# Kernel tuning notes

Measured on AMD Instinct MI355X. Metric: run time of the kernel, lower is better.

Reference implementation:

```python
import jax, jax.numpy as jnp
import numpy as np

EPS = 1e-7            # keras.backend.epsilon()
NEG = -1e30           # log-space 'zero' (avoid -inf for NaN-free grads)
SUB_SAMPLE = (2, 2)   # encoder conv subsampling factors (non-tensor forward arg)


def setup_inputs() -> dict:
    key = jax.random.key(0)
    k1, k2, k3, k4 = jax.random.split(key, 4)
    B, T, C, L = 128, 2000, 128, 200
    logits = jax.random.normal(k1, (B, T, C), jnp.float32)
    y_pred = jax.nn.softmax(logits, axis=-1)  # ctc_batch_cost expects probabilities
    labels = jax.random.randint(k2, (B, L), 0, C - 1, jnp.int32)  # never the blank (C-1)
    # raw frame counts; after two /2 subsamplings -> in [1000, 2000] <= T
    feat_lens = jax.random.randint(k3, (B,), 4000, 8000, jnp.int32)
    label_lens = jax.random.randint(k4, (B,), 50, L + 1, jnp.int32)
    return {"y_pred": y_pred, "labels": labels, "feat_lens": feat_lens, "label_lens": label_lens}


def _ctc_batch_cost(y_pred, labels, feat_lens, label_lens):
    """Faithful reimplementation of keras.backend.ctc_batch_cost (blank = C-1),
    with the CTCLayer's subsampling of feat_lens applied first."""
    for sub in SUB_SAMPLE:
        if sub > 1:
            feat_lens = (feat_lens + 1) // sub
    log_probs = jnp.log(y_pred + EPS)                 # [B,T,C]
    B, T, C = y_pred.shape
    L = labels.shape[1]
    S = 2 * L + 1
    blank = C - 1

    # extended label sequence: blank, l1, blank, l2, ..., blank  -> [B,S]
    ext = jnp.full((B, S), blank, jnp.int32).at[:, 1::2].set(labels)
    # skip transition s-2 -> s allowed iff ext[s] != blank and ext[s] != ext[s-2]
    skip_ok = jnp.concatenate(
        [jnp.zeros((B, 2), bool), (ext[:, 2:] != blank) & (ext[:, 2:] != ext[:, :-2])],
        axis=1,
    )
    bidx = jnp.arange(B)
    i1 = 2 * label_lens - 1   # last non-blank state
    i2 = 2 * label_lens       # trailing blank state

    lp = jnp.swapaxes(log_probs, 0, 1)                # [T,B,C], scan over time

    emit0 = jnp.take_along_axis(lp[0], ext, axis=1)   # [B,S]
    alpha0 = (jnp.full((B, S), NEG, jnp.float32)
              .at[:, 0].set(emit0[:, 0])
              .at[:, 1].set(emit0[:, 1]))
    ll0 = jnp.logaddexp(alpha0[bidx, i1], alpha0[bidx, i2])
    final0 = jnp.where(feat_lens == 1, ll0, NEG)

    def step(carry, inp):
        alpha, final = carry
        t, lp_t = inp
        emit = jnp.take_along_axis(lp_t, ext, axis=1)              # [B,S]
        a1 = jnp.pad(alpha, ((0, 0), (1, 0)), constant_values=NEG)[:, :-1]
        a2 = jnp.pad(alpha, ((0, 0), (2, 0)), constant_values=NEG)[:, :-2]
        m = jnp.logaddexp(alpha, a1)
        m = jnp.where(skip_ok, jnp.logaddexp(m, a2), m)
        alpha = m + emit
        ll = jnp.logaddexp(alpha[bidx, i1], alpha[bidx, i2])
        final = jnp.where(t == feat_lens - 1, ll, final)           # capture at last valid frame
        return (alpha, final), None

    (_, final), _ = jax.lax.scan(step, (alpha0, final0), (jnp.arange(1, T), lp[1:]))
    return -final[:, None]                                          # [B,1] like ctc_batch_cost


def reference(y_pred, labels, feat_lens, label_lens):
    return _ctc_batch_cost(y_pred, labels, feat_lens, label_lens)
```

## Files before the change

kernel.cpp:

```cpp
#include <hip/hip_runtime.h>
#include <math.h>

#define EPSQ 1e-7f
#define TDIM 2000
#define CDIM 128
#define LDIM 200
#define SDIM 401
#define SPL  7
#define SENTE (-(1 << 30))

#define RINGA 0
#define RINGB 8192
#define LABSI 16384
#define PRODA 16592
#define CONSA 16593
#define PRODB 16594
#define CONSB 16595
#define BDONE 16596
#define BVALS 16608
#define BEXPI 17056
#define SMEMN 17120

__device__ __forceinline__ float dpp_shr_f(float x) {
    return __int_as_float(__builtin_amdgcn_update_dpp(0, __float_as_int(x), 0x138, 0xf, 0xf, true));
}
__device__ __forceinline__ int dpp_shr_i(int x) {
    return __builtin_amdgcn_update_dpp(0, x, 0x138, 0xf, 0xf, true);
}
__device__ __forceinline__ float dpp_shl_f(float x) {
    return __int_as_float(__builtin_amdgcn_update_dpp(0, __float_as_int(x), 0x130, 0xf, 0xf, true));
}
__device__ __forceinline__ int dpp_shl_i(int x) {
    return __builtin_amdgcn_update_dpp(0, x, 0x130, 0xf, 0xf, true);
}

__device__ __forceinline__ void renorm_alpha(float a[SPL], int& E, float& fprev, int lane) {
    float mx = fmaxf(fmaxf(fmaxf(a[0], a[1]), fmaxf(a[2], a[3])),
                     fmaxf(fmaxf(a[4], a[5]), a[6]));
    bool zero = (mx == 0.f);
    int e = ((__float_as_int(mx) >> 23) & 0xff) - 127;
    int S_self = zero ? SENTE : (E + e);
    int S1 = dpp_shr_i(S_self);
    if (lane == 0) S1 = SENTE;
    int S2 = dpp_shr_i(S1);
    if (lane == 0) S2 = SENTE;
    int E_new = max(S_self, S1);
    int E_prevnew = max(S1, S2);
    int dg = E - E_new;
    float g = (zero || dg < -126) ? 0.f : __int_as_float((dg + 127) << 23);
#pragma unroll
    for (int j = 0; j < SPL; ++j) a[j] *= g;
    E = E_new;
    int df = E_prevnew - E_new;
    bool fz = (E_prevnew <= SENTE / 2) || (df < -126);
    if (df > 126) df = 126;
    fprev = fz ? 0.f : __int_as_float((df + 127) << 23);
}

__device__ __forceinline__ void renorm_beta(float b[SPL], int& E, float& fnext, int lane) {
    float mx = fmaxf(fmaxf(fmaxf(b[0], b[1]), fmaxf(b[2], b[3])),
                     fmaxf(fmaxf(b[4], b[5]), b[6]));
    bool zero = (mx == 0.f);
    int e = ((__float_as_int(mx) >> 23) & 0xff) - 127;
    int S_self = zero ? SENTE : (E + e);
    int S1 = dpp_shl_i(S_self);
    if (lane == 63) S1 = SENTE;
    int S2 = dpp_shl_i(S1);
    if (lane == 63) S2 = SENTE;
    int E_new = max(S_self, S1);
    int E_nextnew = max(S1, S2);
    int dg = E - E_new;
    float g = (zero || dg < -126) ? 0.f : __int_as_float((dg + 127) << 23);
#pragma unroll
    for (int j = 0; j < SPL; ++j) b[j] *= g;
    E = E_new;
    int df = E_nextnew - E_new;
    bool fz = (E_nextnew <= SENTE / 2) || (df < -126);
    if (df > 126) df = 126;
    fnext = fz ? 0.f : __int_as_float((df + 127) << 23);
}

#define A_STEP(TOFF) do {                                                     \
    float p6 = dpp_shr_f(a[6]) * fprev;                                       \
    float p5 = dpp_shr_f(a[5]) * fprev;                                       \
    float n0 = fmaf(skipf[0], p5,   a[0] + p6)   * q[(1+(TOFF))&3][0];        \
    float n1 = fmaf(skipf[1], p6,   a[1] + a[0]) * q[(1+(TOFF))&3][1];        \
    float n2 = fmaf(skipf[2], a[0], a[2] + a[1]) * q[(1+(TOFF))&3][2];        \
    float n3 = fmaf(skipf[3], a[1], a[3] + a[2]) * q[(1+(TOFF))&3][3];        \
    float n4 = fmaf(skipf[4], a[2], a[4] + a[3]) * q[(1+(TOFF))&3][4];        \
    float n5 = fmaf(skipf[5], a[3], a[5] + a[4]) * q[(1+(TOFF))&3][5];        \
    float n6 = fmaf(skipf[6], a[4], a[6] + a[5]) * q[(1+(TOFF))&3][6];        \
    a[0]=n0; a[1]=n1; a[2]=n2; a[3]=n3; a[4]=n4; a[5]=n5; a[6]=n6;            \
    if (t + (TOFF) == m) {                                                    \
        _Pragma("unroll")                                                     \
        for (int j = 0; j < SPL; ++j) ac[j] = a[j];                           \
        Eac = E;                                                              \
    }                                                                         \
    {   const int rr = ((t + (TOFF) + 2) & 63) << 7;                          \
        _Pragma("unroll")                                                     \
        for (int j = 0; j < SPL; ++j)                                         \
            q[(3+(TOFF))&3][j] = ringA[rr + cls[j]];                          \
    }                                                                         \
} while (0);

#define B_STEP(SOFF) do {                                                     \
    float c0 = bb[0]*q[(SOFF)&3][0], c1 = bb[1]*q[(SOFF)&3][1];               \
    float c2 = bb[2]*q[(SOFF)&3][2], c3 = bb[3]*q[(SOFF)&3][3];               \
    float c4 = bb[4]*q[(SOFF)&3][4], c5 = bb[5]*q[(SOFF)&3][5];               \
    float c6 = bb[6]*q[(SOFF)&3][6];                                          \
    float cn0 = dpp_shl_f(c0) * fnext;                                        \
    float cn1 = dpp_shl_f(c1) * fnext;                                        \
    bb[0] = fmaf(skb[0], c2, c0 + c1);                                        \
    bb[1] = fmaf(skb[1], c3, c1 + c2);                                        \
    bb[2] = fmaf(skb[2], c4, c2 + c3);                                        \
    bb[3] = fmaf(skb[3], c5, c3 + c4);                                        \
    bb[4] = fmaf(skb[4], c6, c4 + c5);                                        \
    bb[5] = fmaf(skb[5], cn0, c5 + c6);                                       \
    bb[6] = fmaf(skb[6], cn1, c6 + cn0);                                      \
    if (s + (SOFF) == scap) {                                                 \
        _Pragma("unroll")                                                     \
        for (int j = 0; j < SPL; ++j) bc[j] = bb[j];                          \
        Ebc = E;                                                              \
    }                                                                         \
    {   const int rr = ((t0 - s - (SOFF) - 2) & 63) << 7;                     \
        _Pragma("unroll")                                                     \
        for (int j = 0; j < SPL; ++j)                                         \
            q[(2+(SOFF))&3][j] = ringB[rr + cls[j]];                          \
    }                                                                         \
} while (0);

__global__ void __launch_bounds__(256, 1)
__attribute__((amdgpu_waves_per_eu(1, 1)))
ctc_kernel(const float* __restrict__ y_pred,
           const int* __restrict__ labels,
           const int* __restrict__ feat_lens,
           const int* __restrict__ label_lens,
           float* __restrict__ out)
{
    __shared__ int smem[SMEMN];
    float* smf = (float*)smem;
    volatile int* vsm = (volatile int*)smem;

    const int b = blockIdx.x;
    const int tid = threadIdx.x;
    const int lane = tid & 63;
    const int wv = tid >> 6;

    int f = feat_lens[b];
    f = (f + 1) >> 1; f = (f + 1) >> 1;
    const int Tbm1 = f - 1;
    const int m = f >> 1;

    if (tid < 8) smem[PRODA + tid] = 0;
    const int* labrow = labels + b * LDIM;
    for (int i = tid; i < LDIM; i += 256) smem[LABSI + i] = labrow[i];
    __syncthreads();

    const float4* rp4 = (const float4*)(y_pred + (size_t)b * TDIM * CDIM);

    if (wv == 2) {
        const int pend = (m + 18) >> 1;
        int p = 0;
        while (p <= pend) {
            while (vsm[CONSA] + 32 < p + 8) __builtin_amdgcn_s_sleep(2);
            asm volatile("" ::: "memory");
            float4 w[8];
#pragma unroll
            for (int i = 0; i < 8; ++i) {
                int pi = p + i; if (pi > pend) pi = pend;
                w[i] = rp4[pi * 64 + lane];
            }
#pragma unroll
            for (int i = 0; i < 8; ++i) {
                int pi = p + i; if (pi > pend) pi = pend;
                float4 x = w[i];
                x.x += EPSQ; x.y += EPSQ; x.z += EPSQ; x.w += EPSQ;
                *(float4*)&smf[RINGA + (pi & 31) * 256 + lane * 4] = x;
            }
            asm volatile("s_waitcnt lgkmcnt(0)" ::: "memory");
            vsm[PRODA] = p + 8;
            p += 8;
        }
        return;
    }
    if (wv == 3) {
        const int pstart = Tbm1 >> 1;
        int pl = (m - 18) >> 1; if (pl < 0) pl = 0;
        const int kend = pstart - pl;
        int k = 0;
        while (k <= kend) {
            while (vsm[CONSB] + 32 < k + 8) __builtin_amdgcn_s_sleep(2);
            asm volatile("" ::: "memory");
            float4 w[8];
#pragma unroll
            for (int i = 0; i < 8; ++i) {
                int ki = k + i; if (ki > kend) ki = kend;
                w[i] = rp4[(pstart - ki) * 64 + lane];
            }
#pragma unroll
            for (int i = 0; i < 8; ++i) {
                int ki = k + i; if (ki > kend) ki = kend;
                float4 x = w[i];
                x.x += EPSQ; x.y += EPSQ; x.z += EPSQ; x.w += EPSQ;
                *(float4*)&smf[RINGB + ((pstart - ki) & 31) * 256 + lane * 4] = x;
            }
            asm volatile("s_waitcnt lgkmcnt(0)" ::: "memory");
            vsm[PRODB] = k + 8;
            k += 8;
        }
        return;
    }

    const int llen = label_lens[b];
    const int i1 = 2 * llen - 1, i2 = 2 * llen;
    int cls[SPL]; float skipf[SPL];
    const int s0 = lane * SPL;
#pragma unroll
    for (int j = 0; j < SPL; ++j) {
        int s = s0 + j;
        int c = CDIM - 1; float sk = 0.f;
        if (s < SDIM && (s & 1)) {
            int kk = s >> 1;
            c = smem[LABSI + kk];
            if (kk >= 1 && smem[LABSI + kk] != smem[LABSI + kk - 1]) sk = 1.f;
        }
        cls[j] = c; skipf[j] = sk;
    }
    const float* ringA = &smf[RINGA];
    const float* ringB = &smf[RINGB];

    if (wv == 0) {
        float a[SPL], q[4][SPL], ac[SPL];
        int E = 0, Eac = 0;
        float fprev = 0.f;
#pragma unroll
        for (int j = 0; j < SPL; ++j) { a[j] = 0.f; ac[j] = 0.f; }

        while (vsm[PRODA] < 2) __builtin_amdgcn_s_sleep(1);
        asm volatile("" ::: "memory");
#pragma unroll
        for (int j = 0; j < SPL; ++j) {
            q[0][j] = ringA[(0 << 7) + cls[j]];
            q[1][j] = ringA[(1 << 7) + cls[j]];
            q[2][j] = ringA[(2 << 7) + cls[j]];
        }
        if (lane == 0) { a[0] = q[0][0]; a[1] = q[0][1]; }

        int t = 1;
        while (t <= m) {
            vsm[CONSA] = (t >= 2) ? (((t - 2) >> 1) + 1) : 0;
            int need = ((t + 17) >> 1) + 1;
            while (vsm[PRODA] < need) __builtin_amdgcn_s_sleep(1);
            asm volatile("" ::: "memory");
            renorm_alpha(a, E, fprev, lane);
            A_STEP(0) A_STEP(1) A_STEP(2) A_STEP(3)
            renorm_alpha(a, E, fprev, lane);
            A_STEP(4) A_STEP(5) A_STEP(6) A_STEP(7)
            renorm_alpha(a, E, fprev, lane);
            A_STEP(8) A_STEP(9) A_STEP(10) A_STEP(11)
            renorm_alpha(a, E, fprev, lane);
            A_STEP(12) A_STEP(13) A_STEP(14) A_STEP(15)
            t += 16;
        }
        vsm[CONSA] = 1 << 28;
        asm volatile("" ::: "memory");

        while (vsm[BDONE] == 0) __builtin_amdgcn_s_sleep(1);
        asm volatile("" ::: "memory");
        int Eb = smem[BEXPI + lane];
        float dot = 0.f;
#pragma unroll
        for (int j = 0; j < SPL; ++j)
            dot = fmaf(ac[j], smf[BVALS + lane * SPL + j], dot);
        float l2 = (dot > 0.f) ? (log2f(dot) + (float)(Eac + Eb)) : -1e30f;
        float M = l2;
#pragma unroll
        for (int d = 1; d < 64; d <<= 1) M = fmaxf(M, __shfl_xor(M, d, 64));
        float S = exp2f(l2 - M);
#pragma unroll
        for (int d = 1; d < 64; d <<= 1) S += __shfl_xor(S, d, 64);
        if (lane == 0)
            out[b] = -(M + log2f(S)) * 0.69314718055994530942f;
    } else {
        float bb[SPL], q[4][SPL], bc[SPL];
        int E = 0, Ebc = 0;
        float fnext = 0.f;
#pragma unroll
        for (int j = 0; j < SPL; ++j) {
            int s = s0 + j;
            bb[j] = (s == i1 || s == i2) ? 1.f : 0.f;
            bc[j] = 0.f;
        }
        float skb[SPL];
#pragma unroll
        for (int j = 0; j < 5; ++j) skb[j] = skipf[j + 2];
        skb[5] = (lane == 63) ? 0.f : __shfl_down(skipf[0], 1, 64);
        skb[6] = (lane == 63) ? 0.f : __shfl_down(skipf[1], 1, 64);

        const int t0 = Tbm1;
        const int nb = t0 - m;
        const int scap = nb - 1;
        const int pstart = t0 >> 1;

        while (vsm[PRODB] < 2) __builtin_amdgcn_s_sleep(1);
        asm volatile("" ::: "memory");
#pragma unroll
        for (int j = 0; j < SPL; ++j) {
            q[0][j] = ringB[((t0 & 63) << 7) + cls[j]];
            q[1][j] = ringB[(((t0 - 1) & 63) << 7) + cls[j]];
        }

        int s = 0;
        while (s < nb) {
            int tcur = t0 - s;
            vsm[CONSB] = pstart - ((tcur + 2) >> 1) + 1;
            int need = pstart - ((tcur - 17) >> 1) + 1;
            while (vsm[PRODB] < need) __builtin_amdgcn_s_sleep(1);
            asm volatile("" ::: "memory");
            renorm_beta(bb, E, fnext, lane);
            B_STEP(0) B_STEP(1) B_STEP(2) B_STEP(3)
            renorm_beta(bb, E, fnext, lane);
            B_STEP(4) B_STEP(5) B_STEP(6) B_STEP(7)
            renorm_beta(bb, E, fnext, lane);
            B_STEP(8) B_STEP(9) B_STEP(10) B_STEP(11)
            renorm_beta(bb, E, fnext, lane);
            B_STEP(12) B_STEP(13) B_STEP(14) B_STEP(15)
            s += 16;
        }
        vsm[CONSB] = 1 << 28;
        asm volatile("" ::: "memory");
#pragma unroll
        for (int j = 0; j < SPL; ++j) smf[BVALS + lane * SPL + j] = bc[j];
        smem[BEXPI + lane] = Ebc;
        asm volatile("s_waitcnt lgkmcnt(0)" ::: "memory");
        vsm[BDONE] = 1;
    }
}

extern "C" void kernel_launch(void* const* d_in, const int* in_sizes, int n_in,
                              void* d_out, int out_size, void* d_ws, size_t ws_size,
                              hipStream_t stream) {
    (void)d_ws; (void)ws_size; (void)n_in; (void)out_size;
    const float* y_pred     = (const float*)d_in[0];
    const int*   labels     = (const int*)d_in[1];
    const int*   feat_lens  = (const int*)d_in[2];
    const int*   label_lens = (const int*)d_in[3];
    float* out = (float*)d_out;
    const int B = in_sizes[2];
    ctc_kernel<<<B, 256, 0, stream>>>(y_pred, labels, feat_lens, label_lens, out);
}
```

Measured before the change: 273.3 us.

## Split alpha and beta passes into separate blocks with a combine kernel

```diff
diff --git a/kernel.cpp b/kernel.cpp
--- a/kernel.cpp
+++ b/kernel.cpp
@@ -5,21 +5,15 @@
 #define TDIM 2000
 #define CDIM 128
 #define LDIM 200
-#define SDIM 401
 #define SPL  7
 #define SENTE (-(1 << 30))
 
-#define RINGA 0
-#define RINGB 8192
+#define RING  0
 #define LABSI 16384
-#define PRODA 16592
-#define CONSA 16593
-#define PRODB 16594
-#define CONSB 16595
-#define BDONE 16596
-#define BVALS 16608
-#define BEXPI 17056
-#define SMEMN 17120
+#define PRODF 16584
+#define CONSF 16585
+#define SMEMN 16592
+
 
 __device__ __forceinline__ float dpp_shr_f(float x) {
     return __int_as_float(__builtin_amdgcn_update_dpp(0, __float_as_int(x), 0x138, 0xf, 0xf, true));
@@ -96,10 +90,10 @@
         for (int j = 0; j < SPL; ++j) ac[j] = a[j];                           \
         Eac = E;                                                              \
     }                                                                         \
-    {   const int rr = ((t + (TOFF) + 2) & 63) << 7;                          \
+    {   const int rr = ((t + (TOFF) + 3) & 127) << 7;                         \
         _Pragma("unroll")                                                     \
         for (int j = 0; j < SPL; ++j)                                         \
-            q[(3+(TOFF))&3][j] = ringA[rr + cls[j]];                          \
+            q[(TOFF)&3][j] = ring[rr + cls[j]];                               \
     }                                                                         \
 } while (0);
 
@@ -122,26 +116,48 @@
         for (int j = 0; j < SPL; ++j) bc[j] = bb[j];                          \
         Ebc = E;                                                              \
     }                                                                         \
-    {   const int rr = ((t0 - s - (SOFF) - 2) & 63) << 7;                     \
+    {   const int rr = ((t0 - s - (SOFF) - 3) & 127) << 7;                    \
         _Pragma("unroll")                                                     \
         for (int j = 0; j < SPL; ++j)                                         \
-            q[(2+(SOFF))&3][j] = ringB[rr + cls[j]];                          \
+            q[(3+(SOFF))&3][j] = ring[rr + cls[j]];                           \
     }                                                                         \
 } while (0);
 
-__global__ void __launch_bounds__(256, 1)
+#define LOADG(W, G) do {                                                      \
+    _Pragma("unroll")                                                         \
+    for (int i_ = 0; i_ < 8; ++i_) {                                          \
+        int ii_ = (G) * 8 + i_; if (ii_ > iend) ii_ = iend;                   \
+        int pr_ = role ? (pbase - ii_) : ii_;                                 \
+        W[i_] = rp4[pr_ * 64 + lane];                                         \
+    }                                                                         \
+} while (0)
+
+#define STOREG(W, G) do {                                                     \
+    _Pragma("unroll")                                                         \
+    for (int i_ = 0; i_ < 8; ++i_) {                                          \
+        int ii_ = (G) * 8 + i_; if (ii_ > iend) ii_ = iend;                   \
+        int pr_ = role ? (pbase - ii_) : ii_;                                 \
+        float4 x_ = W[i_];                                                    \
+        x_.x += EPSQ; x_.y += EPSQ; x_.z += EPSQ; x_.w += EPSQ;               \
+        *(float4*)&smf[RING + (pr_ & 63) * 256 + lane * 4] = x_;              \
+    }                                                                         \
+} while (0)
+
+__global__ void __launch_bounds__(128, 1)
 __attribute__((amdgpu_waves_per_eu(1, 1)))
 ctc_kernel(const float* __restrict__ y_pred,
            const int* __restrict__ labels,
            const int* __restrict__ feat_lens,
            const int* __restrict__ label_lens,
-           float* __restrict__ out)
+           float* __restrict__ ws)
 {
     __shared__ int smem[SMEMN];
     float* smf = (float*)smem;
     volatile int* vsm = (volatile int*)smem;
 
-    const int b = blockIdx.x;
+    const int bid = blockIdx.x;
+    const int b = bid >> 1;
+    const int role = bid & 1;
     const int tid = threadIdx.x;
     const int lane = tid & 63;
     const int wv = tid >> 6;
@@ -151,62 +167,41 @@
     const int Tbm1 = f - 1;
     const int m = f >> 1;
 
-    if (tid < 8) smem[PRODA + tid] = 0;
+    if (tid < 2) smem[PRODF + tid] = 0;
     const int* labrow = labels + b * LDIM;
-    for (int i = tid; i < LDIM; i += 256) smem[LABSI + i] = labrow[i];
+    for (int i = tid; i < LDIM; i += 128) smem[LABSI + i] = labrow[i];
     __syncthreads();
 
     const float4* rp4 = (const float4*)(y_pred + (size_t)b * TDIM * CDIM);
 
-    if (wv == 2) {
-        const int pend = (m + 18) >> 1;
-        int p = 0;
-        while (p <= pend) {
-            while (vsm[CONSA] + 32 < p + 8) __builtin_amdgcn_s_sleep(2);
+    if (wv == 1) {
+        int iend, pbase;
+        if (role == 0) { iend = (m + 18) >> 1; pbase = 0; }
+        else {
+            const int pstart = Tbm1 >> 1;
+            int pl = (m - 18) >> 1; if (pl < 0) pl = 0;
+            iend = pstart - pl; pbase = pstart;
+        }
+        const int ng = (iend >> 3) + 1;
+        float4 w0[8], w1[8];
+        LOADG(w0, 0);
+        if (ng > 1) LOADG(w1, 1);
+        int g = 0;
+        while (true) {
+            while (vsm[CONSF] + 64 < 8 * (g + 1)) __builtin_amdgcn_s_sleep(2);
             asm volatile("" ::: "memory");
-            float4 w[8];
-#pragma unroll
-            for (int i = 0; i < 8; ++i) {
-                int pi = p + i; if (pi > pend) pi = pend;
-                w[i] = rp4[pi * 64 + lane];
-            }
-#pragma unroll
-            for (int i = 0; i < 8; ++i) {
-                int pi = p + i; if (pi > pend) pi = pend;
-                float4 x = w[i];
-                x.x += EPSQ; x.y += EPSQ; x.z += EPSQ; x.w += EPSQ;
-                *(float4*)&smf[RINGA + (pi & 31) * 256 + lane * 4] = x;
-            }
+            STOREG(w0, g);
             asm volatile("s_waitcnt lgkmcnt(0)" ::: "memory");
-            vsm[PRODA] = p + 8;
-            p += 8;
-        }
-        return;
-    }
-    if (wv == 3) {
-        const int pstart = Tbm1 >> 1;
-        int pl = (m - 18) >> 1; if (pl < 0) pl = 0;
-        const int kend = pstart - pl;
-        int k = 0;
-        while (k <= kend) {
-            while (vsm[CONSB] + 32 < k + 8) __builtin_amdgcn_s_sleep(2);
+            vsm[PRODF] = 8 * (g + 1);
+            if (g + 2 < ng) LOADG(w0, g + 2);
+            ++g; if (g >= ng) break;
+            while (vsm[CONSF] + 64 < 8 * (g + 1)) __builtin_amdgcn_s_sleep(2);
             asm volatile("" ::: "memory");
-            float4 w[8];
-#pragma unroll
-            for (int i = 0; i < 8; ++i) {
-                int ki = k + i; if (ki > kend) ki = kend;
-                w[i] = rp4[(pstart - ki) * 64 + lane];
-            }
-#pragma unroll
-            for (int i = 0; i < 8; ++i) {
-                int ki = k + i; if (ki > kend) ki = kend;
-                float4 x = w[i];
-                x.x += EPSQ; x.y += EPSQ; x.z += EPSQ; x.w += EPSQ;
-                *(float4*)&smf[RINGB + ((pstart - ki) & 31) * 256 + lane * 4] = x;
-            }
+            STOREG(w1, g);
             asm volatile("s_waitcnt lgkmcnt(0)" ::: "memory");
-            vsm[PRODB] = k + 8;
-            k += 8;
+            vsm[PRODF] = 8 * (g + 1);
+            if (g + 2 < ng) LOADG(w1, g + 2);
+            ++g; if (g >= ng) break;
         }
         return;
     }
@@ -219,38 +214,38 @@
     for (int j = 0; j < SPL; ++j) {
         int s = s0 + j;
         int c = CDIM - 1; float sk = 0.f;
-        if (s < SDIM && (s & 1)) {
+        if (s < (2 * LDIM + 1) && (s & 1)) {
             int kk = s >> 1;
             c = smem[LABSI + kk];
             if (kk >= 1 && smem[LABSI + kk] != smem[LABSI + kk - 1]) sk = 1.f;
         }
         cls[j] = c; skipf[j] = sk;
     }
-    const float* ringA = &smf[RINGA];
-    const float* ringB = &smf[RINGB];
-
-    if (wv == 0) {
+    const float* ring = &smf[RING];
+
+    if (role == 0) {
         float a[SPL], q[4][SPL], ac[SPL];
         int E = 0, Eac = 0;
         float fprev = 0.f;
 #pragma unroll
         for (int j = 0; j < SPL; ++j) { a[j] = 0.f; ac[j] = 0.f; }
 
-        while (vsm[PRODA] < 2) __builtin_amdgcn_s_sleep(1);
+        while (vsm[PRODF] < 2) __builtin_amdgcn_s_sleep(1);
         asm volatile("" ::: "memory");
 #pragma unroll
         for (int j = 0; j < SPL; ++j) {
-            q[0][j] = ringA[(0 << 7) + cls[j]];
-            q[1][j] = ringA[(1 << 7) + cls[j]];
-            q[2][j] = ringA[(2 << 7) + cls[j]];
+            q[0][j] = ring[(0 << 7) + cls[j]];
+            q[1][j] = ring[(1 << 7) + cls[j]];
+            q[2][j] = ring[(2 << 7) + cls[j]];
+            q[3][j] = ring[(3 << 7) + cls[j]];
         }
         if (lane == 0) { a[0] = q[0][0]; a[1] = q[0][1]; }
 
         int t = 1;
         while (t <= m) {
-            vsm[CONSA] = (t >= 2) ? (((t - 2) >> 1) + 1) : 0;
-            int need = ((t + 17) >> 1) + 1;
-            while (vsm[PRODA] < need) __builtin_amdgcn_s_sleep(1);
+            vsm[CONSF] = (t >= 2) ? (((t - 2) >> 1) + 1) : 0;
+            int need = ((t + 18) >> 1) + 1;
+            while (vsm[PRODF] < need) __builtin_amdgcn_s_sleep(1);
             asm volatile("" ::: "memory");
             renorm_alpha(a, E, fprev, lane);
             A_STEP(0) A_STEP(1) A_STEP(2) A_STEP(3)
@@ -262,25 +257,12 @@
             A_STEP(12) A_STEP(13) A_STEP(14) A_STEP(15)
             t += 16;
         }
-        vsm[CONSA] = 1 << 28;
+        vsm[CONSF] = 1 << 28;
         asm volatile("" ::: "memory");
-
-        while (vsm[BDONE] == 0) __builtin_amdgcn_s_sleep(1);
-        asm volatile("" ::: "memory");
-        int Eb = smem[BEXPI + lane];
-        float dot = 0.f;
-#pragma unroll
-        for (int j = 0; j < SPL; ++j)
-            dot = fmaf(ac[j], smf[BVALS + lane * SPL + j], dot);
-        float l2 = (dot > 0.f) ? (log2f(dot) + (float)(Eac + Eb)) : -1e30f;
-        float M = l2;
-#pragma unroll
-        for (int d = 1; d < 64; d <<= 1) M = fmaxf(M, __shfl_xor(M, d, 64));
-        float S = exp2f(l2 - M);
-#pragma unroll
-        for (int d = 1; d < 64; d <<= 1) S += __shfl_xor(S, d, 64);
-        if (lane == 0)
-            out[b] = -(M + log2f(S)) * 0.69314718055994530942f;
+        float* wsb = ws + (size_t)b * 1024;
+#pragma unroll
+        for (int j = 0; j < SPL; ++j) wsb[lane * SPL + j] = ac[j];
+        ((int*)wsb)[448 + lane] = Eac;
     } else {
         float bb[SPL], q[4][SPL], bc[SPL];
         int E = 0, Ebc = 0;
@@ -302,20 +284,22 @@
         const int scap = nb - 1;
         const int pstart = t0 >> 1;
 
-        while (vsm[PRODB] < 2) __builtin_amdgcn_s_sleep(1);
+        while (vsm[PRODF] < 2) __builtin_amdgcn_s_sleep(1);
         asm volatile("" ::: "memory");
 #pragma unroll
         for (int j = 0; j < SPL; ++j) {
-            q[0][j] = ringB[((t0 & 63) << 7) + cls[j]];
-            q[1][j] = ringB[(((t0 - 1) & 63) << 7) + cls[j]];
+            q[0][j] = ring[((t0 & 127) << 7) + cls[j]];
+            q[1][j] = ring[(((t0 - 1) & 127) << 7) + cls[j]];
+            q[2][j] = ring[(((t0 - 2) & 127) << 7) + cls[j]];
+            q[3][j] = 0.f;
         }
 
         int s = 0;
         while (s < nb) {
             int tcur = t0 - s;
-            vsm[CONSB] = pstart - ((tcur + 2) >> 1) + 1;
-            int need = pstart - ((tcur - 17) >> 1) + 1;
-            while (vsm[PRODB] < need) __builtin_amdgcn_s_sleep(1);
+            vsm[CONSF] = pstart - ((tcur + 2) >> 1) + 1;
+            int need = pstart - ((tcur - 18) >> 1) + 1;
+            while (vsm[PRODF] < need) __builtin_amdgcn_s_sleep(1);
             asm volatile("" ::: "memory");
             renorm_beta(bb, E, fnext, lane);
             B_STEP(0) B_STEP(1) B_STEP(2) B_STEP(3)
@@ -327,25 +311,49 @@
             B_STEP(12) B_STEP(13) B_STEP(14) B_STEP(15)
             s += 16;
         }
-        vsm[CONSB] = 1 << 28;
+        vsm[CONSF] = 1 << 28;
         asm volatile("" ::: "memory");
-#pragma unroll
-        for (int j = 0; j < SPL; ++j) smf[BVALS + lane * SPL + j] = bc[j];
-        smem[BEXPI + lane] = Ebc;
-        asm volatile("s_waitcnt lgkmcnt(0)" ::: "memory");
-        vsm[BDONE] = 1;
+        float* wsb = ws + (size_t)b * 1024 + 512;
+#pragma unroll
+        for (int j = 0; j < SPL; ++j) wsb[lane * SPL + j] = bc[j];
+        ((int*)wsb)[448 + lane] = Ebc;
     }
+}
+
+__global__ void __launch_bounds__(64, 1)
+ctc_combine(const float* __restrict__ ws, float* __restrict__ out)
+{
+    const int b = blockIdx.x;
+    const int lane = threadIdx.x & 63;
+    const float* wa = ws + (size_t)b * 1024;
+    const float* wb = wa + 512;
+    const int Ea = ((const int*)wa)[448 + lane];
+    const int Eb = ((const int*)wb)[448 + lane];
+    float dot = 0.f;
+#pragma unroll
+    for (int j = 0; j < SPL; ++j)
+        dot = fmaf(wa[lane * SPL + j], wb[lane * SPL + j], dot);
+    float l2 = (dot > 0.f) ? (log2f(dot) + (float)(Ea + Eb)) : -1e30f;
+    float M = l2;
+#pragma unroll
+    for (int d = 1; d < 64; d <<= 1) M = fmaxf(M, __shfl_xor(M, d, 64));
+    float S = exp2f(l2 - M);
+#pragma unroll
+    for (int d = 1; d < 64; d <<= 1) S += __shfl_xor(S, d, 64);
+    if (lane == 0) out[b] = -(M + log2f(S)) * 0.69314718055994530942f;
 }
 
 extern "C" void kernel_launch(void* const* d_in, const int* in_sizes, int n_in,
                               void* d_out, int out_size, void* d_ws, size_t ws_size,
                               hipStream_t stream) {
-    (void)d_ws; (void)ws_size; (void)n_in; (void)out_size;
+    (void)n_in; (void)out_size; (void)ws_size;
     const float* y_pred     = (const float*)d_in[0];
     const int*   labels     = (const int*)d_in[1];
     const int*   feat_lens  = (const int*)d_in[2];
     const int*   label_lens = (const int*)d_in[3];
     float* out = (float*)d_out;
+    float* ws  = (float*)d_ws;
     const int B = in_sizes[2];
-    ctc_kernel<<<B, 256, 0, stream>>>(y_pred, labels, feat_lens, label_lens, out);
-}
+    ctc_kernel<<<B * 2, 128, 0, stream>>>(y_pred, labels, feat_lens, label_lens, ws);
+    ctc_combine<<<B, 64, 0, stream>>>(ws, out);
+}
```

Measured after the change: 271.5 us. Within noise of the previous version (-0.6%).
